# Performance work log

Measured on AMD Instinct MI355X. Metric: run time of the kernel, lower is better.

Reference implementation:

```python
import jax, jax.numpy as jnp
import numpy as np

NUM_USERS = 100000
NUM_ITEMS = 100000
EMB_DIM = 64
NUM_NODES = NUM_USERS + NUM_ITEMS
NUM_EDGES = 4000000
BATCH = 4096
NUM_LAYERS = 2


def setup_inputs() -> dict:
    key = jax.random.key(0)
    ks = jax.random.split(key, 8)
    user = jax.random.randint(ks[0], (BATCH,), 0, NUM_USERS, dtype=jnp.int64) if jax.config.jax_enable_x64 else jax.random.randint(ks[0], (BATCH,), 0, NUM_USERS, dtype=jnp.int32)
    pos = jax.random.randint(ks[1], (BATCH,), 0, NUM_ITEMS, dtype=jnp.int32)
    neg = jax.random.randint(ks[2], (BATCH,), 0, NUM_ITEMS, dtype=jnp.int32)
    edge_row = jax.random.randint(ks[3], (NUM_EDGES,), 0, NUM_NODES, dtype=jnp.int32)
    edge_col = jax.random.randint(ks[4], (NUM_EDGES,), 0, NUM_NODES, dtype=jnp.int32)
    # normalized adjacency values (degree-normalized in real LightGCN)
    edge_val = jax.random.uniform(ks[5], (NUM_EDGES,), dtype=jnp.float32) * 0.01
    user_emb = jax.random.normal(ks[6], (NUM_USERS, EMB_DIM), dtype=jnp.float32) * 0.01
    item_emb = jax.random.normal(ks[7], (NUM_ITEMS, EMB_DIM), dtype=jnp.float32) * 0.01
    return {"user": user, "pos": pos, "neg": neg,
            "edge_row": edge_row, "edge_col": edge_col, "edge_val": edge_val,
            "user_emb": user_emb, "item_emb": item_emb}


def _spmm(edge_row, edge_col, edge_val, x):
    # out[r] = sum_e val[e] * x[col[e]]  -- sparse adjacency times dense emb
    msgs = edge_val[:, None] * x[edge_col]  # [E, D]
    return jax.ops.segment_sum(msgs, edge_row, num_segments=NUM_NODES)


def reference(user, pos, neg, edge_row, edge_col, edge_val, user_emb, item_emb):
    all_emb = jnp.concatenate([user_emb, item_emb], axis=0)  # [N, D]
    acc = all_emb
    h = all_emb
    for _ in range(NUM_LAYERS):
        h = _spmm(edge_row, edge_col, edge_val, h)
        acc = acc + h
    lightgcn_out = acc / (NUM_LAYERS + 1)  # mean over stacked layer embeddings
    u = lightgcn_out[:NUM_USERS]
    i = lightgcn_out[NUM_USERS:]
    user_latent = u[user]          # [B, D]
    positive_latent = i[pos]       # [B, D]
    negative_latent = i[neg]       # [B, D]
    positive_score = jnp.sum(user_latent * positive_latent, axis=1)
    negative_score = jnp.sum(user_latent * negative_latent, axis=1)
    return positive_score, negative_score
```

## Files before the change

### kernel.cpp

```cpp
#include <hip/hip_runtime.h>
#include <cstdint>
#include <cstddef>

#define NUM_USERS 100000
#define NUM_ITEMS 100000
#define NUM_NODES 200000
#define NUM_EDGES 4000000
#define BATCH     4096
#define EMB       64

#define NB    782
#define CAP   5632
#define CHUNK 16384
#define PTHREADS 1024
#define EPB   16
#define RPT   11
#define NWORDS 6250


__device__ __forceinline__ unsigned short f2bf(float f) {
    unsigned u = __float_as_uint(f);
    u = (u + 0x7FFFu + ((u >> 16) & 1u)) >> 16;
    return (unsigned short)u;
}
__device__ __forceinline__ float bf2f(unsigned short b) {
    return __uint_as_float(((unsigned)b) << 16);
}


__global__ void k_part1(const int* __restrict__ user, const int* __restrict__ pos,
                        const int* __restrict__ neg,
                        const int* __restrict__ erow, const int* __restrict__ ecol,
                        const float* __restrict__ eval_,
                        const float* __restrict__ uemb, const float* __restrict__ iemb,
                        unsigned short* __restrict__ xb,
                        int* __restrict__ bcur,
                        unsigned* __restrict__ memb, unsigned* __restrict__ need,
                        int2* __restrict__ tmp) {
    __shared__ int hist[NB];
    __shared__ int base[NB];
    int t = threadIdx.x;
    int gid = blockIdx.x * PTHREADS + t;
    for (int i = t; i < NB; i += PTHREADS) hist[i] = 0;

    const int TOT8 = (NUM_NODES * EMB) / 8;
    const size_t UELEMS = (size_t)NUM_USERS * EMB;
    for (int i = gid; i < TOT8; i += gridDim.x * PTHREADS) {
        size_t off = (size_t)i * 8;
        const float* src = (off < UELEMS) ? (uemb + off) : (iemb + (off - UELEMS));
        float4 f0 = ((const float4*)src)[0];
        float4 f1 = ((const float4*)src)[1];
        ((ushort4*)(xb + off))[0] = make_ushort4(f2bf(f0.x), f2bf(f0.y), f2bf(f0.z), f2bf(f0.w));
        ((ushort4*)(xb + off))[1] = make_ushort4(f2bf(f1.x), f2bf(f1.y), f2bf(f1.z), f2bf(f1.w));
    }
    if (gid < 3 * BATCH) {
        int b = gid & (BATCH - 1);
        int w = gid >> 12;
        int node = (w == 0) ? user[b] : (w == 1) ? (NUM_USERS + pos[b]) : (NUM_USERS + neg[b]);
        unsigned bit = 1u << (node & 31);
        atomicOr(&memb[node >> 5], bit);
        atomicOr(&need[node >> 5], bit);
    }
    __syncthreads();

    int start = blockIdx.x * CHUNK;
    int rows[EPB], ranks[EPB];
#pragma unroll
    for (int k = 0; k < EPB; ++k) {
        int e = start + t + k * PTHREADS;
        if (e < NUM_EDGES) {
            int r = erow[e];
            rows[k]  = r;
            ranks[k] = atomicAdd(&hist[r >> 8], 1);
        } else {
            rows[k] = -1;
        }
    }
    __syncthreads();
    for (int i = t; i < NB; i += PTHREADS) {
        int c = hist[i];
        base[i] = c ? atomicAdd(&bcur[i], c) : 0;
    }
    __syncthreads();
#pragma unroll
    for (int k = 0; k < EPB; ++k) {
        int e = start + t + k * PTHREADS;
        if (rows[k] >= 0) {
            int r   = rows[k];
            int bkt = r >> 8;
            int rel = base[bkt] + ranks[k];
            if (rel < CAP)
                tmp[bkt * CAP + rel] = make_int2(((r & 255) << 24) | ecol[e], __float_as_int(eval_[e]));
        }
    }
}


__global__ void k_part2(const int* __restrict__ bcur, const int2* __restrict__ tmp,
                        const unsigned* __restrict__ memb,
                        int2* __restrict__ epack, int2* __restrict__ rowext,
                        unsigned* __restrict__ need) {
    __shared__ int cnt[256];
    __shared__ int sc[256];
    __shared__ int loc[256];
    __shared__ unsigned mw[8];
    int b = blockIdx.x, t = threadIdx.x;
    int base_row = b << 8;
    int nrows = min(256, NUM_NODES - base_row);
    int s0 = b * CAP;
    int n = min(bcur[b], CAP);
    if (t < 256) cnt[t] = 0;
    if (t < 8) {
        int wi = (base_row >> 5) + t;
        mw[t] = (wi < NWORDS) ? memb[wi] : 0u;
    }
    __syncthreads();
    int2 r[RPT];
#pragma unroll
    for (int i = 0; i < RPT; ++i) {
        int idx = t + i * 512;
        if (idx < n) {
            r[i] = tmp[s0 + idx];
            atomicAdd(&cnt[((unsigned)r[i].x) >> 24], 1);
        }
    }
    __syncthreads();
    int v = 0;
    if (t < 256) { v = cnt[t]; sc[t] = v; }
    __syncthreads();
    for (int off = 1; off < 256; off <<= 1) {
        int add = 0;
        if (t < 256 && t >= off) add = sc[t - off];
        __syncthreads();
        if (t < 256 && t >= off) sc[t] += add;
        __syncthreads();
    }
    if (t < 256) {
        int cur = s0 + sc[t] - v;
        if (t < nrows) rowext[base_row + t] = make_int2(cur, v);
        loc[t] = cur;
    }
    __syncthreads();
#pragma unroll
    for (int i = 0; i < RPT; ++i) {
        int idx = t + i * 512;
        if (idx < n) {
            int2 rec = r[i];
            unsigned rl = ((unsigned)rec.x) >> 24;
            int p = atomicAdd(&loc[rl], 1);
            int col = rec.x & 0xFFFFFF;
            epack[p] = make_int2(col, rec.y);
            if ((mw[rl >> 5] >> (rl & 31)) & 1u)
                atomicOr(&need[col >> 5], 1u << (col & 31));
        }
    }
}


__global__ void k_spmm1(const int2* __restrict__ rowext, const int2* __restrict__ epack,
                        const unsigned short* __restrict__ xb,
                        const unsigned* __restrict__ need,
                        unsigned short* __restrict__ h1) {
    int wid  = (blockIdx.x * blockDim.x + threadIdx.x) >> 6;
    int lane = threadIdx.x & 63;
    if (wid >= NUM_NODES) return;
    if (!((need[wid >> 5] >> (wid & 31)) & 1u)) return;
    int g = lane >> 4;
    int q = (lane & 15) * 4;
    int2 se = rowext[wid];
    int s = se.x, t = se.x + se.y;
    float a0 = 0.f, a1 = 0.f, a2 = 0.f, a3 = 0.f;
    int e = s;
    int tfull = s + ((t - s) & ~7);
    for (; e < tfull; e += 8) {
        int2 pA = epack[e + g];
        int2 pB = epack[e + 4 + g];
        float vA = __int_as_float(pA.y);
        float vB = __int_as_float(pB.y);
        ushort4 xA = *(const ushort4*)(xb + (size_t)pA.x * EMB + q);
        ushort4 xB = *(const ushort4*)(xb + (size_t)pB.x * EMB + q);
        a0 = fmaf(vA, bf2f(xA.x), a0); a1 = fmaf(vA, bf2f(xA.y), a1);
        a2 = fmaf(vA, bf2f(xA.z), a2); a3 = fmaf(vA, bf2f(xA.w), a3);
        a0 = fmaf(vB, bf2f(xB.x), a0); a1 = fmaf(vB, bf2f(xB.y), a1);
        a2 = fmaf(vB, bf2f(xB.z), a2); a3 = fmaf(vB, bf2f(xB.w), a3);
    }
    if (e < t) {
        int eA = e + g, eB = e + 4 + g;
        int2 pA = epack[eA < t ? eA : s];
        int2 pB = epack[eB < t ? eB : s];
        float vA = (eA < t) ? __int_as_float(pA.y) : 0.f;
        float vB = (eB < t) ? __int_as_float(pB.y) : 0.f;
        ushort4 xA = *(const ushort4*)(xb + (size_t)pA.x * EMB + q);
        ushort4 xB = *(const ushort4*)(xb + (size_t)pB.x * EMB + q);
        a0 = fmaf(vA, bf2f(xA.x), a0); a1 = fmaf(vA, bf2f(xA.y), a1);
        a2 = fmaf(vA, bf2f(xA.z), a2); a3 = fmaf(vA, bf2f(xA.w), a3);
        a0 = fmaf(vB, bf2f(xB.x), a0); a1 = fmaf(vB, bf2f(xB.y), a1);
        a2 = fmaf(vB, bf2f(xB.z), a2); a3 = fmaf(vB, bf2f(xB.w), a3);
    }
    a0 += __shfl_xor(a0, 16, 64); a1 += __shfl_xor(a1, 16, 64);
    a2 += __shfl_xor(a2, 16, 64); a3 += __shfl_xor(a3, 16, 64);
    a0 += __shfl_xor(a0, 32, 64); a1 += __shfl_xor(a1, 32, 64);
    a2 += __shfl_xor(a2, 32, 64); a3 += __shfl_xor(a3, 32, 64);
    if (lane < 16) {
        ushort4 o = make_ushort4(f2bf(a0), f2bf(a1), f2bf(a2), f2bf(a3));
        *(ushort4*)(h1 + (size_t)wid * EMB + q) = o;
    }
}


__device__ __forceinline__ const float* node_ptr(int c, const float* __restrict__ uemb,
                                                 const float* __restrict__ iemb) {
    return (c < NUM_USERS) ? (uemb + (size_t)c * EMB)
                           : (iemb + (size_t)(c - NUM_USERS) * EMB);
}

__global__ void k_final(const int* __restrict__ user, const int* __restrict__ pos,
                        const int* __restrict__ neg,
                        const int2* __restrict__ rowext, const int2* __restrict__ epack,
                        const float* __restrict__ uemb, const float* __restrict__ iemb,
                        const unsigned short* __restrict__ h1, float* __restrict__ out) {
    __shared__ float lds[3 * EMB];
    int b    = blockIdx.x;
    int w    = threadIdx.x >> 6;
    int lane = threadIdx.x & 63;
    int g = lane >> 4;
    int q = (lane & 15) * 4;

    int node;
    if (w == 0)      node = user[b];
    else if (w == 1) node = NUM_USERS + pos[b];
    else             node = NUM_USERS + neg[b];

    int2 se = rowext[node];
    int s = se.x, t = se.x + se.y;
    float a0 = 0.f, a1 = 0.f, a2 = 0.f, a3 = 0.f;
    for (int e = s; e < t; e += 8) {
        int eA = e + g, eB = e + 4 + g;
        int2 pA = epack[eA < t ? eA : s];
        int2 pB = epack[eB < t ? eB : s];
        float vA = (eA < t) ? __int_as_float(pA.y) : 0.f;
        float vB = (eB < t) ? __int_as_float(pB.y) : 0.f;
        ushort4 yA = *(const ushort4*)(h1 + (size_t)pA.x * EMB + q);
        ushort4 yB = *(const ushort4*)(h1 + (size_t)pB.x * EMB + q);
        a0 = fmaf(vA, bf2f(yA.x), a0); a1 = fmaf(vA, bf2f(yA.y), a1);
        a2 = fmaf(vA, bf2f(yA.z), a2); a3 = fmaf(vA, bf2f(yA.w), a3);
        a0 = fmaf(vB, bf2f(yB.x), a0); a1 = fmaf(vB, bf2f(yB.y), a1);
        a2 = fmaf(vB, bf2f(yB.z), a2); a3 = fmaf(vB, bf2f(yB.w), a3);
    }
    a0 += __shfl_xor(a0, 16, 64); a1 += __shfl_xor(a1, 16, 64);
    a2 += __shfl_xor(a2, 16, 64); a3 += __shfl_xor(a3, 16, 64);
    a0 += __shfl_xor(a0, 32, 64); a1 += __shfl_xor(a1, 32, 64);
    a2 += __shfl_xor(a2, 32, 64); a3 += __shfl_xor(a3, 32, 64);

    if (lane < 16) {
        const float* xbp = node_ptr(node, uemb, iemb) + q;
        float4  xd = *(const float4*)xbp;
        ushort4 hn = *(const ushort4*)(h1 + (size_t)node * EMB + q);
        a0 = (a0 + xd.x + bf2f(hn.x)) / 3.0f;
        a1 = (a1 + xd.y + bf2f(hn.y)) / 3.0f;
        a2 = (a2 + xd.z + bf2f(hn.z)) / 3.0f;
        a3 = (a3 + xd.w + bf2f(hn.w)) / 3.0f;
        *(float4*)(lds + w * EMB + q) = make_float4(a0, a1, a2, a3);
    }
    __syncthreads();

    if (w < 2) {
        float prod = lds[lane] * lds[(w + 1) * EMB + lane];
        for (int off = 32; off; off >>= 1) prod += __shfl_xor(prod, off, 64);
        if (lane == 0) out[w * BATCH + b] = prod;
    }
}


extern "C" void kernel_launch(void* const* d_in, const int* in_sizes, int n_in,
                              void* d_out, int out_size, void* d_ws, size_t ws_size,
                              hipStream_t stream) {
    const int*   user  = (const int*)d_in[0];
    const int*   pos   = (const int*)d_in[1];
    const int*   neg   = (const int*)d_in[2];
    const int*   erow  = (const int*)d_in[3];
    const int*   ecol  = (const int*)d_in[4];
    const float* eval_ = (const float*)d_in[5];
    const float* uemb  = (const float*)d_in[6];
    const float* iemb  = (const float*)d_in[7];
    float* out = (float*)d_out;

    char* ws = (char*)d_ws;
    unsigned short* xb = (unsigned short*)(ws);
    unsigned short* h1 = (unsigned short*)(ws + 25600000);
    int2* tmp      = (int2*)(ws + 25600000);
    int2* rowext   = (int2*)(ws + 60833792);
    int*  bcur     = (int*)(ws + 62433792);
    unsigned* memb = (unsigned*)(ws + 62436920);
    unsigned* need = (unsigned*)(ws + 62461920);
    int2* epack    = (int2*)(ws + 62486920);

    hipMemsetAsync(ws + 62433792, 0, 53128, stream);

    k_part1<<<(NUM_EDGES + CHUNK - 1) / CHUNK, PTHREADS, 0, stream>>>(
        user, pos, neg, erow, ecol, eval_, uemb, iemb, xb, bcur, memb, need, tmp);

    k_part2<<<NB, 512, 0, stream>>>(bcur, tmp, memb, epack, rowext, need);

    k_spmm1<<<(NUM_NODES * 64 + 255) / 256, 256, 0, stream>>>(rowext, epack, xb, need, h1);

    k_final<<<BATCH, 192, 0, stream>>>(user, pos, neg, rowext, epack,
                                       uemb, iemb, h1, out);
}
```

Before: 345.2 us.

## Stage bucketed edges in LDS for coalesced writes and use wider buckets

The partition kernel now sorts each chunk's edge records by bucket in shared memory, using a local prefix scan, before writing them out. One wave per bucket then copies that bucket's records as a contiguous, coalesced run into the global temp buffer, replacing scattered per-edge writes. Buckets double to 512 rows each (391 buckets), the record packing shifts to an 18-bit column and a 9-bit local row, and the second pass runs 1024 threads per block. In exchange the partition kernel needs 64KB of shared memory per block, which limits occupancy, and it adds a scan plus an extra barrier phase.

```diff
diff --git a/kernel.cpp b/kernel.cpp
--- a/kernel.cpp
+++ b/kernel.cpp
@@ -9,11 +9,11 @@
 #define BATCH     4096
 #define EMB       64
 
-#define NB    782
-#define CAP   5632
-#define CHUNK 16384
+#define NB    391
+#define CAP   11264
+#define CHUNK 8192
 #define PTHREADS 1024
-#define EPB   16
+#define EPB   8
 #define RPT   11
 #define NWORDS 6250
 
@@ -37,11 +37,13 @@
                         int* __restrict__ bcur,
                         unsigned* __restrict__ memb, unsigned* __restrict__ need,
                         int2* __restrict__ tmp) {
-    __shared__ int hist[NB];
-    __shared__ int base[NB];
+    __shared__ int  hist[NB];
+    __shared__ int  sst[512];
+    __shared__ int  gb[NB];
+    __shared__ int2 srec[CHUNK];
     int t = threadIdx.x;
     int gid = blockIdx.x * PTHREADS + t;
-    for (int i = t; i < NB; i += PTHREADS) hist[i] = 0;
+    if (t < NB) hist[t] = 0;
 
     const int TOT8 = (NUM_NODES * EMB) / 8;
     const size_t UELEMS = (size_t)NUM_USERS * EMB;
@@ -71,26 +73,46 @@
         if (e < NUM_EDGES) {
             int r = erow[e];
             rows[k]  = r;
-            ranks[k] = atomicAdd(&hist[r >> 8], 1);
+            ranks[k] = atomicAdd(&hist[r >> 9], 1);
         } else {
             rows[k] = -1;
         }
     }
     __syncthreads();
-    for (int i = t; i < NB; i += PTHREADS) {
-        int c = hist[i];
-        base[i] = c ? atomicAdd(&bcur[i], c) : 0;
-    }
-    __syncthreads();
+
+    if (t < 512) sst[t] = (t < NB) ? hist[t] : 0;
+    __syncthreads();
+    for (int off = 1; off < 512; off <<= 1) {
+        int add = 0;
+        if (t < 512 && t >= off) add = sst[t - off];
+        __syncthreads();
+        if (t < 512 && t >= off) sst[t] += add;
+        __syncthreads();
+    }
+    if (t < NB) gb[t] = atomicAdd(&bcur[t], hist[t]);
+
 #pragma unroll
     for (int k = 0; k < EPB; ++k) {
-        int e = start + t + k * PTHREADS;
         if (rows[k] >= 0) {
+            int e   = start + t + k * PTHREADS;
             int r   = rows[k];
-            int bkt = r >> 8;
-            int rel = base[bkt] + ranks[k];
+            int bkt = r >> 9;
+            int lp  = sst[bkt] - hist[bkt] + ranks[k];
+            srec[lp] = make_int2(((r & 511) << 18) | ecol[e], __float_as_int(eval_[e]));
+        }
+    }
+    __syncthreads();
+
+    int wv = t >> 6, ln = t & 63;
+    for (int bkt = wv; bkt < NB; bkt += 16) {
+        int c  = hist[bkt];
+        int st = sst[bkt] - c;
+        int g0 = gb[bkt];
+        size_t base = (size_t)bkt * CAP;
+        for (int j = ln; j < c; j += 64) {
+            int rel = g0 + j;
             if (rel < CAP)
-                tmp[bkt * CAP + rel] = make_int2(((r & 255) << 24) | ecol[e], __float_as_int(eval_[e]));
+                tmp[base + rel] = srec[st + j];
         }
     }
 }
@@ -100,17 +122,17 @@
                         const unsigned* __restrict__ memb,
                         int2* __restrict__ epack, int2* __restrict__ rowext,
                         unsigned* __restrict__ need) {
-    __shared__ int cnt[256];
-    __shared__ int sc[256];
-    __shared__ int loc[256];
-    __shared__ unsigned mw[8];
+    __shared__ int cnt[512];
+    __shared__ int sc[512];
+    __shared__ int loc[512];
+    __shared__ unsigned mw[16];
     int b = blockIdx.x, t = threadIdx.x;
-    int base_row = b << 8;
-    int nrows = min(256, NUM_NODES - base_row);
+    int base_row = b << 9;
+    int nrows = min(512, NUM_NODES - base_row);
     int s0 = b * CAP;
     int n = min(bcur[b], CAP);
-    if (t < 256) cnt[t] = 0;
-    if (t < 8) {
+    if (t < 512) cnt[t] = 0;
+    if (t < 16) {
         int wi = (base_row >> 5) + t;
         mw[t] = (wi < NWORDS) ? memb[wi] : 0u;
     }
@@ -118,24 +140,24 @@
     int2 r[RPT];
 #pragma unroll
     for (int i = 0; i < RPT; ++i) {
-        int idx = t + i * 512;
+        int idx = t + i * 1024;
         if (idx < n) {
             r[i] = tmp[s0 + idx];
-            atomicAdd(&cnt[((unsigned)r[i].x) >> 24], 1);
+            atomicAdd(&cnt[((unsigned)r[i].x) >> 18], 1);
         }
     }
     __syncthreads();
     int v = 0;
-    if (t < 256) { v = cnt[t]; sc[t] = v; }
-    __syncthreads();
-    for (int off = 1; off < 256; off <<= 1) {
+    if (t < 512) { v = cnt[t]; sc[t] = v; }
+    __syncthreads();
+    for (int off = 1; off < 512; off <<= 1) {
         int add = 0;
-        if (t < 256 && t >= off) add = sc[t - off];
+        if (t < 512 && t >= off) add = sc[t - off];
         __syncthreads();
-        if (t < 256 && t >= off) sc[t] += add;
+        if (t < 512 && t >= off) sc[t] += add;
         __syncthreads();
     }
-    if (t < 256) {
+    if (t < 512) {
         int cur = s0 + sc[t] - v;
         if (t < nrows) rowext[base_row + t] = make_int2(cur, v);
         loc[t] = cur;
@@ -143,12 +165,12 @@
     __syncthreads();
 #pragma unroll
     for (int i = 0; i < RPT; ++i) {
-        int idx = t + i * 512;
+        int idx = t + i * 1024;
         if (idx < n) {
             int2 rec = r[i];
-            unsigned rl = ((unsigned)rec.x) >> 24;
+            unsigned rl = ((unsigned)rec.x) >> 18;
             int p = atomicAdd(&loc[rl], 1);
-            int col = rec.x & 0xFFFFFF;
+            int col = rec.x & 0x3FFFF;
             epack[p] = make_int2(col, rec.y);
             if ((mw[rl >> 5] >> (rl & 31)) & 1u)
                 atomicOr(&need[col >> 5], 1u << (col & 31));
@@ -291,16 +313,16 @@
     int2* tmp      = (int2*)(ws + 25600000);
     int2* rowext   = (int2*)(ws + 60833792);
     int*  bcur     = (int*)(ws + 62433792);
-    unsigned* memb = (unsigned*)(ws + 62436920);
-    unsigned* need = (unsigned*)(ws + 62461920);
-    int2* epack    = (int2*)(ws + 62486920);
-
-    hipMemsetAsync(ws + 62433792, 0, 53128, stream);
+    unsigned* memb = (unsigned*)(ws + 62435360);
+    unsigned* need = (unsigned*)(ws + 62460360);
+    int2* epack    = (int2*)(ws + 62485360);
+
+    hipMemsetAsync(ws + 62433792, 0, 51568, stream);
 
     k_part1<<<(NUM_EDGES + CHUNK - 1) / CHUNK, PTHREADS, 0, stream>>>(
         user, pos, neg, erow, ecol, eval_, uemb, iemb, xb, bcur, memb, need, tmp);
 
-    k_part2<<<NB, 512, 0, stream>>>(bcur, tmp, memb, epack, rowext, need);
+    k_part2<<<NB, 1024, 0, stream>>>(bcur, tmp, memb, epack, rowext, need);
 
     k_spmm1<<<(NUM_NODES * 64 + 255) / 256, 256, 0, stream>>>(rowext, epack, xb, need, h1);
 
```

New measurement: 294.6 us. 1.17x faster.
